# Performance work log

Hardware: AMD Instinct MI355X
Metric: run time of the kernel (lower is better)

The kernel has to match this reference:

```python
import jax, jax.numpy as jnp
import numpy as np

NUM_HEADS = 8
ROPE_THETA = 10.0


def _axial_angles(height, width, head_dim, theta):
    # frequencies: 1/theta^(arange(0, head_dim, 4)[:head_dim//4] / head_dim)  -> [head_dim//4]
    hd4 = head_dim // 4
    freqs = 1.0 / (theta ** (np.arange(0, head_dim, 4)[:hd4].astype(np.float32) / head_dim))
    t = np.arange(height * width)
    t_x = (t % width).astype(np.float32)
    t_y = (t // width).astype(np.float32)
    ang_x = np.outer(t_x, freqs)  # [n, head_dim//4]
    ang_y = np.outer(t_y, freqs)
    return jnp.asarray(ang_x), jnp.asarray(ang_y)


def _apply_rope(x, cos, sin):
    # x: [b, h, n, half]; cos/sin: [n, half//2]; complex-pair rotation on last dim
    xr = x[..., 0::2]
    xi = x[..., 1::2]
    out_r = xr * cos - xi * sin
    out_i = xr * sin + xi * cos
    return jnp.stack([out_r, out_i], axis=-1).reshape(x.shape)


def setup_inputs() -> dict:
    key = jax.random.key(0)
    ks = jax.random.split(key, 5)
    b, n, c = 4, 16384, 512
    x = jax.random.normal(ks[0], (b, n, c), dtype=jnp.float32)
    w_qkv = jax.random.normal(ks[1], (c, 3 * c), dtype=jnp.float32) * 0.02
    b_qkv = jax.random.normal(ks[2], (3 * c,), dtype=jnp.float32) * 0.02
    w_proj = jax.random.normal(ks[3], (c, c), dtype=jnp.float32) * 0.02
    b_proj = jax.random.normal(ks[4], (c,), dtype=jnp.float32) * 0.02
    return {"x": x, "w_qkv": w_qkv, "b_qkv": b_qkv, "w_proj": w_proj, "b_proj": b_proj,
            "height": 128, "width": 128}


def reference(x, w_qkv, b_qkv, w_proj, b_proj, height, width):
    b, n, c = x.shape
    h = NUM_HEADS
    hd = c // h
    half = hd // 2

    qkv = (x @ w_qkv + b_qkv).reshape(b, n, 3, h, hd).transpose(2, 0, 3, 1, 4)
    q, k, v = qkv[0], qkv[1], qkv[2]  # each [b, h, n, hd]

    ang_x, ang_y = _axial_angles(height, width, hd, ROPE_THETA)
    cx, sx = jnp.cos(ang_x), jnp.sin(ang_x)
    cy, sy = jnp.cos(ang_y), jnp.sin(ang_y)

    q = jnp.concatenate([_apply_rope(q[..., :half], cx, sx),
                         _apply_rope(q[..., half:], cy, sy)], axis=-1)
    k = jnp.concatenate([_apply_rope(k[..., :half], cx, sx),
                         _apply_rope(k[..., half:], cy, sy)], axis=-1)

    # kernel feature map: elu(x) + 1 (positive)
    q = jax.nn.elu(q) + 1.0
    k = jax.nn.elu(k) + 1.0

    # linear attention: O(n d^2)
    kv = jnp.einsum('bhnd,bhne->bhde', k, v)
    out = jnp.einsum('bhnd,bhde->bhne', q, kv)
    z = 1.0 / (jnp.einsum('bhnd,bhd->bhn', q, k.sum(axis=2)) + 1e-6)
    out = out * z[..., None]

    out = out.transpose(0, 2, 1, 3).reshape(b, n, c)
    return out @ w_proj + b_proj
```

## Files before the change

kernel.cpp:

```cpp
#include <hip/hip_runtime.h>
#include <math.h>

#define BATCH 4
#define NTOK  16384
#define CDIM  512
#define NH    8
#define HD    64
#define M_ROWS (BATCH*NTOK)
#define KDIM  512

typedef _Float16 f16;
typedef _Float16 f16x8 __attribute__((ext_vector_type(8)));
typedef _Float16 f16x4 __attribute__((ext_vector_type(4)));
typedef _Float16 f16x2 __attribute__((ext_vector_type(2)));
typedef float    f32x4 __attribute__((ext_vector_type(4)));

__device__ __forceinline__ void load_lds16(const void* g, void* l) {
    __builtin_amdgcn_global_load_lds(
        (const __attribute__((address_space(1))) void*)g,
        (__attribute__((address_space(3))) void*)l, 16, 0, 0);
}

__global__ void rope_tables(float* __restrict__ tab) {
    int tid = threadIdx.x;
    for (int i = 0; i < 16; i++) {
        int idx = tid + i * 256;
        int t   = (idx >> 4) & 127;
        int fi  = idx & 15;
        double freq = pow(10.0, -(double)fi / 16.0);
        double ang  = (double)t * freq;
        tab[idx * 2]     = (float)cos(ang);
        tab[idx * 2 + 1] = (float)sin(ang);
    }
}

__global__ void convert_x_f16(const float* __restrict__ in, f16* __restrict__ outp) {
    int i = blockIdx.x * 256 + threadIdx.x;
    float4 a = *(const float4*)&in[(size_t)i * 8];
    float4 b = *(const float4*)&in[(size_t)i * 8 + 4];
    f16x8 o;
    o[0]=(f16)a.x; o[1]=(f16)a.y; o[2]=(f16)a.z; o[3]=(f16)a.w;
    o[4]=(f16)b.x; o[5]=(f16)b.y; o[6]=(f16)b.z; o[7]=(f16)b.w;
    *(f16x8*)&outp[(size_t)i * 8] = o;
}

template<int PERM>
__global__ void convert_wT(const float* __restrict__ w, f16* __restrict__ wt, int N) {
    int idx = blockIdx.x * 256 + threadIdx.x;
    int n = idx >> 9, k = idx & 511;
    int tc = n;
    if (PERM) {
        int blk = n >> 5, pos = n & 31;
        tc = blk * 32 + ((pos < 16) ? (pos * 2) : ((pos - 16) * 2 + 1));
    }
    wt[idx] = (f16)w[(size_t)k * N + tc];
}

template<int MODE>
__global__ __launch_bounds__(256, 2)
void gemm_f16(const f16* __restrict__ A, const f16* __restrict__ Bt,
              const float* __restrict__ bias,
              float* __restrict__ Co,
              f16* __restrict__ qd, f16* __restrict__ kd, f16* __restrict__ vd,
              const float* __restrict__ tab, int ncol_tiles)
{
    __shared__ f16 As[128 * 64];
    __shared__ f16 Bs[128 * 64];
    const int tid  = threadIdx.x;
    const int lane = tid & 63;
    const int wave = tid >> 6;
    const int wy = wave >> 1, wx = wave & 1;

    const int bid = blockIdx.x;
    const int xcd = bid & 7;
    const int idx = bid >> 3;
    const int ct  = idx % ncol_tiles;
    const int rt  = (idx / ncol_tiles) * 8 + xcd;
    const int row0 = rt * 128;
    const int col0 = ct * 128;

    const int l15 = lane & 15;
    const int l4  = lane >> 4;

    f32x4 acc[4][4];
    #pragma unroll
    for (int mt = 0; mt < 4; mt++)
        #pragma unroll
        for (int nt = 0; nt < 4; nt++)
            acc[mt][nt] = (f32x4){0.f, 0.f, 0.f, 0.f};

    const int pbase = wave * 256;

    for (int k0 = 0; k0 < KDIM; k0 += 64) {
        #pragma unroll
        for (int i = 0; i < 4; i++) {
            int p  = pbase + i * 64 + lane;
            int m  = p >> 3;
            int jp = p & 7;
            int j  = jp ^ (m & 7);
            load_lds16(&A [(size_t)(row0 + m) * KDIM + k0 + j * 8],
                       &As[(pbase + i * 64) * 8]);
            load_lds16(&Bt[(size_t)(col0 + m) * KDIM + k0 + j * 8],
                       &Bs[(pbase + i * 64) * 8]);
        }
        __syncthreads();

        #pragma unroll
        for (int s = 0; s < 2; s++) {
            f16x8 af[4], bf[4];
            #pragma unroll
            for (int t = 0; t < 4; t++) {
                int ra = wy * 64 + t * 16 + l15;
                int rb = wx * 64 + t * 16 + l15;
                int ca = ((s << 2) | l4) ^ (ra & 7);
                int cb = ((s << 2) | l4) ^ (rb & 7);
                af[t] = *(const f16x8*)&As[ra * 64 + ca * 8];
                bf[t] = *(const f16x8*)&Bs[rb * 64 + cb * 8];
            }
            #pragma unroll
            for (int mt = 0; mt < 4; mt++)
                #pragma unroll
                for (int nt = 0; nt < 4; nt++)
                    acc[mt][nt] = __builtin_amdgcn_mfma_f32_16x16x32_f16(af[mt], bf[nt], acc[mt][nt], 0, 0, 0);
        }
        __syncthreads();
    }

    if (MODE == 0) {
        #pragma unroll
        for (int q = 0; q < 2; q++) {
            int B32 = (col0 + wx * 64 + q * 32) >> 5;
            int t0c = B32 * 32 + 2 * l15;
            float bv0 = bias[t0c];
            float bv1 = bias[t0c + 1];
            #pragma unroll
            for (int mt = 0; mt < 4; mt++)
                #pragma unroll
                for (int r = 0; r < 4; r++) {
                    int row = row0 + wy * 64 + mt * 16 + l4 * 4 + r;
                    float2 o2;
                    o2.x = acc[mt][2 * q][r]     + bv0;
                    o2.y = acc[mt][2 * q + 1][r] + bv1;
                    *(float2*)&Co[(size_t)row * CDIM + t0c] = o2;
                }
        }
    } else {
        const int which = col0 >> 9;
        f16* dst = (which == 0) ? qd : (which == 1) ? kd : vd;
        const float2* tab2 = (const float2*)tab;
        #pragma unroll
        for (int q = 0; q < 2; q++) {
            int B32  = (col0 + wx * 64 + q * 32) >> 5;
            int t0   = B32 * 32 + 2 * l15;
            int c512 = t0 & 511;
            float bv0 = bias[t0];
            float bv1 = bias[t0 + 1];
            int isy  = B32 & 1;
            const float2* ct = tab2 + isy * 2048 + l15;
            if (which == 2) {
                #pragma unroll
                for (int mt = 0; mt < 4; mt++)
                    #pragma unroll
                    for (int r = 0; r < 4; r++) {
                        int row = row0 + wy * 64 + mt * 16 + l4 * 4 + r;
                        f16x2 pk;
                        pk[0] = (f16)(acc[mt][2 * q][r]     + bv0);
                        pk[1] = (f16)(acc[mt][2 * q + 1][r] + bv1);
                        *(f16x2*)&dst[(size_t)row * CDIM + c512] = pk;
                    }
            } else {
                #pragma unroll
                for (int mt = 0; mt < 4; mt++)
                    #pragma unroll
                    for (int r = 0; r < 4; r++) {
                        int row = row0 + wy * 64 + mt * 16 + l4 * 4 + r;
                        int tok = row & (NTOK - 1);
                        int t   = isy ? (tok >> 7) : (tok & 127);
                        float2 cs = ct[t * 16];
                        float xr = acc[mt][2 * q][r]     + bv0;
                        float xi = acc[mt][2 * q + 1][r] + bv1;
                        float o_r = xr * cs.x - xi * cs.y;
                        float o_i = xr * cs.y + xi * cs.x;
                        o_r = (o_r > 0.f) ? o_r + 1.f : __expf(o_r);
                        o_i = (o_i > 0.f) ? o_i + 1.f : __expf(o_i);
                        f16x2 pk; pk[0] = (f16)o_r; pk[1] = (f16)o_i;
                        *(f16x2*)&dst[(size_t)row * CDIM + c512] = pk;
                    }
            }
        }
    }
}

__global__ __launch_bounds__(256, 4)
void kv_kernel(const f16* __restrict__ kk, const f16* __restrict__ vv,
               float* __restrict__ kvt, float* __restrict__ ksum)
{
    int bh = blockIdx.x;
    int b = bh >> 3, h = bh & 7;
    int t0 = blockIdx.y * 1024;
    __shared__ float ks[64][68];
    __shared__ float vs[64][68];
    int tid = threadIdx.x;
    const int wave = tid >> 6;
    const int lane = tid & 63;
    const int ly = lane >> 3;
    const int lx = lane & 7;
    const int o  = (tid & 7) * 8;

    float acc[8][8];
    float ksacc[8];
    #pragma unroll
    for (int r = 0; r < 8; r++) { ksacc[r] = 0.f;
        #pragma unroll
        for (int j = 0; j < 8; j++) acc[r][j] = 0.f; }

    const size_t rowbase = (size_t)b * NTOK;
    for (int tt = t0; tt < t0 + 1024; tt += 64) {
        #pragma unroll
        for (int i = 0; i < 2; i++) {
            int idx = tid + i * 256;
            int tok = idx >> 3;
            size_t g = (rowbase + tt + tok) * CDIM + h * HD + o;
            f16x8 k8 = *(const f16x8*)&kk[g];
            f16x8 v8 = *(const f16x8*)&vv[g];
            float4 klo = {(float)k8[0], (float)k8[1], (float)k8[2], (float)k8[3]};
            float4 khi = {(float)k8[4], (float)k8[5], (float)k8[6], (float)k8[7]};
            float4 vlo = {(float)v8[0], (float)v8[1], (float)v8[2], (float)v8[3]};
            float4 vhi = {(float)v8[4], (float)v8[5], (float)v8[6], (float)v8[7]};
            *(float4*)&ks[tok][o]     = klo;
            *(float4*)&ks[tok][o + 4] = khi;
            *(float4*)&vs[tok][o]     = vlo;
            *(float4*)&vs[tok][o + 4] = vhi;
            ksacc[0] += klo.x; ksacc[1] += klo.y; ksacc[2] += klo.z; ksacc[3] += klo.w;
            ksacc[4] += khi.x; ksacc[5] += khi.y; ksacc[6] += khi.z; ksacc[7] += khi.w;
        }
        __syncthreads();
        #pragma unroll
        for (int t5 = 0; t5 < 16; t5++) {
            int t = wave * 16 + t5;
            float4 ka0 = *(const float4*)&ks[t][ly * 8];
            float4 ka1 = *(const float4*)&ks[t][ly * 8 + 4];
            float4 va0 = *(const float4*)&vs[t][lx * 8];
            float4 va1 = *(const float4*)&vs[t][lx * 8 + 4];
            float ka[8] = {ka0.x, ka0.y, ka0.z, ka0.w, ka1.x, ka1.y, ka1.z, ka1.w};
            float va[8] = {va0.x, va0.y, va0.z, va0.w, va1.x, va1.y, va1.z, va1.w};
            #pragma unroll
            for (int r = 0; r < 8; r++)
                #pragma unroll
                for (int j = 0; j < 8; j++) acc[r][j] += ka[r] * va[j];
        }
        __syncthreads();
    }

    float* ksl = &vs[0][0];
    {
        float4 a = {ksacc[0], ksacc[1], ksacc[2], ksacc[3]};
        float4 c = {ksacc[4], ksacc[5], ksacc[6], ksacc[7]};
        *(float4*)&ksl[tid * 8]     = a;
        *(float4*)&ksl[tid * 8 + 4] = c;
    }
    float* red = &ks[0][0];
    #pragma unroll
    for (int w = 0; w < 4; w++) {
        if (wave == w) {
            #pragma unroll
            for (int j = 0; j < 8; j++) {
                int base = (lx * 8 + j) * 64 + ly * 8;
                float4 lo = {acc[0][j], acc[1][j], acc[2][j], acc[3][j]};
                float4 hi = {acc[4][j], acc[5][j], acc[6][j], acc[7][j]};
                if (w == 0) {
                    *(float4*)&red[base]     = lo;
                    *(float4*)&red[base + 4] = hi;
                } else {
                    float4 p0 = *(const float4*)&red[base];
                    float4 p1 = *(const float4*)&red[base + 4];
                    p0.x += lo.x; p0.y += lo.y; p0.z += lo.z; p0.w += lo.w;
                    p1.x += hi.x; p1.y += hi.y; p1.z += hi.z; p1.w += hi.w;
                    *(float4*)&red[base]     = p0;
                    *(float4*)&red[base + 4] = p1;
                }
            }
        }
        __syncthreads();
    }
    #pragma unroll
    for (int i = 0; i < 16; i++) {
        int idx = tid + i * 256;
        atomicAdd(&kvt[bh * 4096 + idx], red[idx]);
    }
    if (tid < 64) {
        float s = 0.f;
        #pragma unroll
        for (int m = 0; m < 32; m++)
            s += ksl[((tid >> 3) + m * 8) * 8 + (tid & 7)];
        atomicAdd(&ksum[bh * 64 + tid], s);
    }
}

__global__ void kv_pack(const float* __restrict__ kvt,
                        f16* __restrict__ kvhi, f16* __restrict__ kvlo)
{
    int idx = blockIdx.x * 256 + threadIdx.x;
    float4 v = *(const float4*)&kvt[idx * 4];
    f16x4 hi, lo;
    hi[0] = (f16)v.x; lo[0] = (f16)(v.x - (float)hi[0]);
    hi[1] = (f16)v.y; lo[1] = (f16)(v.y - (float)hi[1]);
    hi[2] = (f16)v.z; lo[2] = (f16)(v.z - (float)hi[2]);
    hi[3] = (f16)v.w; lo[3] = (f16)(v.w - (float)hi[3]);
    *(f16x4*)&kvhi[idx * 4] = hi;
    *(f16x4*)&kvlo[idx * 4] = lo;
}

__global__ __launch_bounds__(256, 4)
void attn_kernel(const f16* __restrict__ q, const f16* __restrict__ kvhi,
                 const f16* __restrict__ kvlo, const float* __restrict__ ksum,
                 f16* __restrict__ attnh)
{
    int bh = blockIdx.x;
    int b = bh >> 3, h = bh & 7;
    int rc = blockIdx.y;
    int tid = threadIdx.x;
    const int lane = tid & 63;
    const int wave = tid >> 6;
    const int l15 = lane & 15;
    const int l4  = lane >> 4;

    f16x8 bhi[2][4], blo[2][4];
    #pragma unroll
    for (int s = 0; s < 2; s++)
        #pragma unroll
        for (int nt = 0; nt < 4; nt++) {
            int e = nt * 16 + l15;
            size_t gb = (size_t)bh * 4096 + e * 64 + s * 32 + l4 * 8;
            bhi[s][nt] = *(const f16x8*)&kvhi[gb];
            blo[s][nt] = *(const f16x8*)&kvlo[gb];
        }
    float ksA[2][8];
    #pragma unroll
    for (int s = 0; s < 2; s++)
        #pragma unroll
        for (int j = 0; j < 8; j++)
            ksA[s][j] = ksum[bh * 64 + s * 32 + l4 * 8 + j];

    const size_t qbase = ((size_t)b * NTOK + rc * 256 + wave * 64) * CDIM + (size_t)h * HD;

    #pragma unroll
    for (int mt = 0; mt < 4; mt++) {
        f16x8 af[2];
        #pragma unroll
        for (int s = 0; s < 2; s++)
            af[s] = *(const f16x8*)&q[qbase + (size_t)(mt * 16 + l15) * CDIM + s * 32 + l4 * 8];

        float zp = 0.f;
        #pragma unroll
        for (int s = 0; s < 2; s++)
            #pragma unroll
            for (int j = 0; j < 8; j++)
                zp += (float)af[s][j] * ksA[s][j];
        zp += __shfl_xor(zp, 16, 64);
        zp += __shfl_xor(zp, 32, 64);
        float zinv = 1.f / (zp + 1e-6f);

        f32x4 acc[4];
        #pragma unroll
        for (int nt = 0; nt < 4; nt++) acc[nt] = (f32x4){0.f, 0.f, 0.f, 0.f};
        #pragma unroll
        for (int s = 0; s < 2; s++)
            #pragma unroll
            for (int nt = 0; nt < 4; nt++) {
                acc[nt] = __builtin_amdgcn_mfma_f32_16x16x32_f16(af[s], bhi[s][nt], acc[nt], 0, 0, 0);
                acc[nt] = __builtin_amdgcn_mfma_f32_16x16x32_f16(af[s], blo[s][nt], acc[nt], 0, 0, 0);
            }

        #pragma unroll
        for (int r = 0; r < 4; r++) {
            float zr = __shfl(zinv, l4 * 4 + r, 64);
            size_t orow = qbase + (size_t)(mt * 16 + l4 * 4 + r) * CDIM;
            #pragma unroll
            for (int nt = 0; nt < 4; nt++)
                attnh[orow + nt * 16 + l15] = (f16)(acc[nt][r] * zr);
        }
    }
}

extern "C" void kernel_launch(void* const* d_in, const int* in_sizes, int n_in,
                              void* d_out, int out_size, void* d_ws, size_t ws_size,
                              hipStream_t stream)
{
    const float* x      = (const float*)d_in[0];
    const float* w_qkv  = (const float*)d_in[1];
    const float* b_qkv  = (const float*)d_in[2];
    const float* w_proj = (const float*)d_in[3];
    const float* b_proj = (const float*)d_in[4];
    float* out = (float*)d_out;
    char*  ws  = (char*)d_ws;

    const size_t NCB = (size_t)M_ROWS * CDIM * sizeof(f16);
    f16*   xh   = (f16*)(ws);
    f16*   qh   = (f16*)(ws + NCB * 1);
    f16*   kh   = (f16*)(ws + NCB * 2);
    f16*   vh   = (f16*)(ws + NCB * 3);
    f16*   wqt  = (f16*)(ws + NCB * 4);
    f16*   wpt  = (f16*)(ws + NCB * 4 + (1536 * 512) * sizeof(f16));
    float* tab  = (float*)(ws + NCB * 4 + (1536 * 512 + 512 * 512) * sizeof(f16));
    float* kvp  = tab + 8192;
    float* ksum = kvp + 32 * 4096;
    f16*   kvhi = (f16*)(ksum + 32 * 64);
    f16*   kvlo = kvhi + 32 * 4096;

    hipMemsetAsync(kvp, 0, (32 * 4096 + 32 * 64) * sizeof(float), stream);
    rope_tables<<<1, 256, 0, stream>>>(tab);
    convert_x_f16<<<M_ROWS * CDIM / 8 / 256, 256, 0, stream>>>(x, xh);
    convert_wT<1><<<1536 * 512 / 256, 256, 0, stream>>>(w_qkv, wqt, 1536);
    convert_wT<1><<<512 * 512 / 256, 256, 0, stream>>>(w_proj, wpt, 512);

    gemm_f16<1><<<6144, 256, 0, stream>>>(xh, wqt, b_qkv,
                                          nullptr, qh, kh, vh, tab, 12);
    kv_kernel<<<dim3(32, 16), 256, 0, stream>>>(kh, vh, kvp, ksum);
    kv_pack<<<128, 256, 0, stream>>>(kvp, kvhi, kvlo);
    attn_kernel<<<dim3(32, 64), 256, 0, stream>>>(qh, kvhi, kvlo, ksum, vh);
    gemm_f16<0><<<2048, 256, 0, stream>>>(vh, wpt, b_proj,
                                          out, nullptr, nullptr, nullptr, nullptr, 4);
}
```

Baseline: 537.9 us.

## Fuse preprocessing kernels into one launch with LDS-tiled weight transpose

Merges the x conversion, both weight transposes and the rope table generation into a single prep kernel that dispatches on block index. This removes three launches and the serial one-block double-precision rope kernel. The weight transpose now goes through a padded 32x32 LDS tile so both reads and writes are coalesced, and the rope table uses float sincosf, which may differ slightly in precision.

```diff
diff --git a/kernel.cpp b/kernel.cpp
--- a/kernel.cpp
+++ b/kernel.cpp
@@ -21,39 +21,52 @@
         (__attribute__((address_space(3))) void*)l, 16, 0, 0);
 }
 
-__global__ void rope_tables(float* __restrict__ tab) {
-    int tid = threadIdx.x;
-    for (int i = 0; i < 16; i++) {
-        int idx = tid + i * 256;
+__global__ __launch_bounds__(256)
+void prep(const float* __restrict__ x, f16* __restrict__ xh,
+          const float* __restrict__ wq, f16* __restrict__ wqt,
+          const float* __restrict__ wp, f16* __restrict__ wpt,
+          float* __restrict__ tab)
+{
+    const int bid = blockIdx.x;
+    const int tid = threadIdx.x;
+    __shared__ float lds[32][33];
+
+    if (bid < 16384) {
+        int i = bid * 256 + tid;
+        float4 a = *(const float4*)&x[(size_t)i * 8];
+        float4 b = *(const float4*)&x[(size_t)i * 8 + 4];
+        f16x8 o;
+        o[0]=(f16)a.x; o[1]=(f16)a.y; o[2]=(f16)a.z; o[3]=(f16)a.w;
+        o[4]=(f16)b.x; o[5]=(f16)b.y; o[6]=(f16)b.z; o[7]=(f16)b.w;
+        *(f16x8*)&xh[(size_t)i * 8] = o;
+    } else if (bid < 16384 + 1024) {
+        int tb = bid - 16384;
+        const float* src; f16* dst; int N;
+        if (tb < 768) { src = wq; dst = wqt; N = 1536; }
+        else          { tb -= 768; src = wp; dst = wpt; N = 512; }
+        int kt  = tb & 15;
+        int ntl = tb >> 4;
+        int tx = tid & 31, ty = tid >> 5;
+        #pragma unroll
+        for (int i = 0; i < 4; i++)
+            lds[ty + 8 * i][tx] = src[(size_t)(kt * 32 + ty + 8 * i) * N + ntl * 32 + tx];
+        __syncthreads();
+        #pragma unroll
+        for (int i = 0; i < 4; i++) {
+            int p  = ty + 8 * i;
+            int tc = (p < 16) ? (2 * p) : (2 * (p - 16) + 1);
+            dst[(size_t)(ntl * 32 + p) * 512 + kt * 32 + tx] = (f16)lds[tx][tc];
+        }
+    } else {
+        int idx = (bid - (16384 + 1024)) * 256 + tid;
         int t   = (idx >> 4) & 127;
         int fi  = idx & 15;
-        double freq = pow(10.0, -(double)fi / 16.0);
-        double ang  = (double)t * freq;
-        tab[idx * 2]     = (float)cos(ang);
-        tab[idx * 2 + 1] = (float)sin(ang);
-    }
-}
-
-__global__ void convert_x_f16(const float* __restrict__ in, f16* __restrict__ outp) {
-    int i = blockIdx.x * 256 + threadIdx.x;
-    float4 a = *(const float4*)&in[(size_t)i * 8];
-    float4 b = *(const float4*)&in[(size_t)i * 8 + 4];
-    f16x8 o;
-    o[0]=(f16)a.x; o[1]=(f16)a.y; o[2]=(f16)a.z; o[3]=(f16)a.w;
-    o[4]=(f16)b.x; o[5]=(f16)b.y; o[6]=(f16)b.z; o[7]=(f16)b.w;
-    *(f16x8*)&outp[(size_t)i * 8] = o;
-}
-
-template<int PERM>
-__global__ void convert_wT(const float* __restrict__ w, f16* __restrict__ wt, int N) {
-    int idx = blockIdx.x * 256 + threadIdx.x;
-    int n = idx >> 9, k = idx & 511;
-    int tc = n;
-    if (PERM) {
-        int blk = n >> 5, pos = n & 31;
-        tc = blk * 32 + ((pos < 16) ? (pos * 2) : ((pos - 16) * 2 + 1));
-    }
-    wt[idx] = (f16)w[(size_t)k * N + tc];
+        float freq = powf(10.f, -(float)fi / 16.f);
+        float s, c;
+        sincosf((float)t * freq, &s, &c);
+        tab[idx * 2]     = c;
+        tab[idx * 2 + 1] = s;
+    }
 }
 
 template<int MODE>
@@ -409,10 +422,7 @@
     f16*   kvlo = kvhi + 32 * 4096;
 
     hipMemsetAsync(kvp, 0, (32 * 4096 + 32 * 64) * sizeof(float), stream);
-    rope_tables<<<1, 256, 0, stream>>>(tab);
-    convert_x_f16<<<M_ROWS * CDIM / 8 / 256, 256, 0, stream>>>(x, xh);
-    convert_wT<1><<<1536 * 512 / 256, 256, 0, stream>>>(w_qkv, wqt, 1536);
-    convert_wT<1><<<512 * 512 / 256, 256, 0, stream>>>(w_proj, wpt, 512);
+    prep<<<16384 + 1024 + 16, 256, 0, stream>>>(x, xh, w_qkv, wqt, w_proj, wpt, tab);
 
     gemm_f16<1><<<6144, 256, 0, stream>>>(xh, wqt, b_qkv,
                                           nullptr, qh, kh, vh, tab, 12);
```

Measured after the change: 537.6 us. Within noise of the previous version (-0.1%).
